# Kernel optimization log

Hardware: AMD Instinct MI355X
Metric: run time of the kernel (lower is better)

## Reference

```python
import jax, jax.numpy as jnp
import numpy as np

N_VERTS = 100000
N_EDGES = 50000
NNZ = 1600000
C_IN = 128
C_OUT = 128


def setup_inputs() -> dict:
    key = jax.random.key(0)
    k = jax.random.split(key, 7)
    X = jax.random.normal(k[0], (N_VERTS, C_IN), dtype=jnp.float32)
    v_ids = jax.random.randint(k[1], (NNZ,), 0, N_VERTS)
    e_ids = jax.random.randint(k[2], (NNZ,), 0, N_EDGES)
    s1 = 1.0 / np.sqrt(C_IN)
    s2 = 1.0 / np.sqrt(C_OUT)
    W_v2e = jax.random.uniform(k[3], (C_IN, C_OUT), jnp.float32, -s1, s1)
    b_v2e = jax.random.uniform(k[4], (C_OUT,), jnp.float32, -s1, s1)
    W_e2v = jax.random.uniform(k[5], (C_OUT, C_OUT), jnp.float32, -s2, s2)
    b_e2v = jax.random.uniform(k[6], (C_OUT,), jnp.float32, -s2, s2)
    return {"X": X, "W_v2e": W_v2e, "b_v2e": b_v2e, "W_e2v": W_e2v,
            "b_e2v": b_e2v, "v_ids": v_ids, "e_ids": e_ids}


def _mean_agg(feats_src, src_ids, dst_ids, num_dst):
    # gather source features along incidence list, segment-mean into destination
    gathered = feats_src[src_ids]                                   # [nnz, C]
    ssum = jax.ops.segment_sum(gathered, dst_ids, num_segments=num_dst)
    cnt = jax.ops.segment_sum(jnp.ones((src_ids.shape[0],), feats_src.dtype),
                              dst_ids, num_segments=num_dst)
    return ssum / jnp.maximum(cnt, 1.0)[:, None]


def reference(X, W_v2e, b_v2e, W_e2v, b_e2v, v_ids, e_ids):
    # theta_v2e
    Xp = X @ W_v2e + b_v2e                                          # [V, C_out]
    # v2e mean aggregation + ReLU
    Y = jax.nn.relu(_mean_agg(Xp, v_ids, e_ids, N_EDGES))           # [E, C_out]
    # theta_e2v
    Yp = Y @ W_e2v + b_e2v                                          # [E, C_out]
    # e2v mean aggregation
    Xo = _mean_agg(Yp, e_ids, v_ids, N_VERTS)                       # [V, C_out]
    # not is_last: final ReLU (bn disabled, dropout in eval mode = identity)
    return jax.nn.relu(Xo)
```

## Files before the change

kernel.cpp:

```cpp
#include <hip/hip_runtime.h>
#include <stdint.h>

#define V_N 100000
#define E_N 50000
#define C_N 128

#define NB_E 196
#define NB_V 391
#define NBINS (NB_E + NB_V)
#define CHUNK 8192
#define CAP_B 10240
#define G1T 782
#define G2T 391

typedef unsigned short u16;
typedef unsigned int u32;

__device__ __forceinline__ u16 f2bf(float f) {
    union { float f; u32 i; } c; c.f = f;
    u32 i = c.i;
    i += 0x7fffu + ((i >> 16) & 1u);
    return (u16)(i >> 16);
}
__device__ __forceinline__ void unpack2(u32 u, float& lo, float& hi) {
    union { u32 i; float f; } a, b;
    a.i = u << 16; b.i = u & 0xffff0000u;
    lo = a.f; hi = b.f;
}

__global__ __launch_bounds__(64) void flagf_k(float* out, float v) {
    if (threadIdx.x == 0 && blockIdx.x == 0) out[0] = v;
}

__global__ __launch_bounds__(256) void zero_i4(int4* __restrict__ p, int n) {
    int i = blockIdx.x * 256 + threadIdx.x;
    if (i < n) { int4 z = {0, 0, 0, 0}; p[i] = z; }
}

template<int MODE>
__device__ __forceinline__ void gemm_body(float* As, float* Wsh, int tile,
                                          const float* __restrict__ A,
                                          const float* __restrict__ W,
                                          const float* __restrict__ bias,
                                          const int* __restrict__ off,
                                          u16* __restrict__ Cout, int M) {
    const int tid = threadIdx.x;
    const int tx = tid & 15;
    const int ty = tid >> 4;
    const int m0 = tile * 128;

    float4 ra[4], rw[4];

    auto loadSlice = [&](int kk) {
        #pragma unroll
        for (int u = 0; u < 4; ++u) {
            int f = tid + u * 256;
            int r = f >> 3, c4 = f & 7;
            float4 val = { 0.f, 0.f, 0.f, 0.f };
            if (m0 + r < M)
                val = *(const float4*)(A + (size_t)(m0 + r) * C_N + kk + c4 * 4);
            ra[u] = val;
            int rwr = f >> 5, cw = f & 31;
            rw[u] = *(const float4*)(W + (size_t)(kk + rwr) * C_N + cw * 4);
        }
    };
    auto writeSlice = [&]() {
        #pragma unroll
        for (int u = 0; u < 4; ++u) {
            int f = tid + u * 256;
            int r = f >> 3, c4 = f & 7;
            int sc4 = c4 ^ ((r >> 3) & 7);
            *(float4*)(As + r * 32 + sc4 * 4) = ra[u];
            int rwr = f >> 5, cw = f & 31;
            *(float4*)(Wsh + rwr * 128 + cw * 4) = rw[u];
        }
    };

    float acc[8][8];
    #pragma unroll
    for (int i = 0; i < 8; ++i)
        #pragma unroll
        for (int j = 0; j < 8; ++j) acc[i][j] = 0.f;

    loadSlice(0);
    writeSlice();
    __syncthreads();

    #pragma unroll 1
    for (int kk = 0; kk < 128; kk += 32) {
        if (kk < 96) loadSlice(kk + 32);
        #pragma unroll
        for (int k4 = 0; k4 < 32; k4 += 4) {
            float4 a[8];
            #pragma unroll
            for (int i = 0; i < 8; ++i) {
                int row = ty * 8 + i;
                int sc4 = (k4 >> 2) ^ (ty & 7);
                a[i] = *(const float4*)(As + row * 32 + sc4 * 4);
            }
            #pragma unroll
            for (int dk = 0; dk < 4; ++dk) {
                float4 w0 = *(const float4*)(Wsh + (k4 + dk) * 128 + tx * 4);
                float4 w1 = *(const float4*)(Wsh + (k4 + dk) * 128 + 64 + tx * 4);
                #pragma unroll
                for (int i = 0; i < 8; ++i) {
                    float av = (dk == 0) ? a[i].x : (dk == 1) ? a[i].y : (dk == 2) ? a[i].z : a[i].w;
                    acc[i][0] = fmaf(av, w0.x, acc[i][0]);
                    acc[i][1] = fmaf(av, w0.y, acc[i][1]);
                    acc[i][2] = fmaf(av, w0.z, acc[i][2]);
                    acc[i][3] = fmaf(av, w0.w, acc[i][3]);
                    acc[i][4] = fmaf(av, w1.x, acc[i][4]);
                    acc[i][5] = fmaf(av, w1.y, acc[i][5]);
                    acc[i][6] = fmaf(av, w1.z, acc[i][6]);
                    acc[i][7] = fmaf(av, w1.w, acc[i][7]);
                }
            }
        }
        if (kk < 96) {
            __syncthreads();
            writeSlice();
            __syncthreads();
        }
    }

    float4 bb0 = *(const float4*)(bias + tx * 4);
    float4 bb1 = *(const float4*)(bias + 64 + tx * 4);
    #pragma unroll
    for (int i = 0; i < 8; ++i) {
        int m = m0 + ty * 8 + i;
        if (m >= M) break;
        float inv = 1.f;
        if (MODE) { int len = off[m + 1] - off[m]; inv = 1.f / (float)max(len, 1); }
        float v0, v1, v2, v3, v4, v5, v6, v7;
        if (MODE) {
            v0 = acc[i][0] * inv + bb0.x; v1 = acc[i][1] * inv + bb0.y;
            v2 = acc[i][2] * inv + bb0.z; v3 = acc[i][3] * inv + bb0.w;
            v4 = acc[i][4] * inv + bb1.x; v5 = acc[i][5] * inv + bb1.y;
            v6 = acc[i][6] * inv + bb1.z; v7 = acc[i][7] * inv + bb1.w;
        } else {
            v0 = acc[i][0] + bb0.x; v1 = acc[i][1] + bb0.y;
            v2 = acc[i][2] + bb0.z; v3 = acc[i][3] + bb0.w;
            v4 = acc[i][4] + bb1.x; v5 = acc[i][5] + bb1.y;
            v6 = acc[i][6] + bb1.z; v7 = acc[i][7] + bb1.w;
        }
        u32 p0 = (u32)f2bf(v0) | ((u32)f2bf(v1) << 16);
        u32 p1 = (u32)f2bf(v2) | ((u32)f2bf(v3) << 16);
        u32 p2 = (u32)f2bf(v4) | ((u32)f2bf(v5) << 16);
        u32 p3 = (u32)f2bf(v6) | ((u32)f2bf(v7) << 16);
        u32* dst = (u32*)(Cout + (size_t)m * C_N);
        uint2 q0 = { p0, p1 }, q1 = { p2, p3 };
        *(uint2*)(dst + tx * 2) = q0;
        *(uint2*)(dst + 32 + tx * 2) = q1;
    }
}

__global__ __launch_bounds__(256) void g1hist_k(const float* __restrict__ X,
                                                const float* __restrict__ W,
                                                const float* __restrict__ bias,
                                                u16* __restrict__ Xp,
                                                const int* __restrict__ v_ids,
                                                const int* __restrict__ e_ids,
                                                int* __restrict__ gbin, int nnz) {
    __shared__ __align__(16) float sm[2][4096];
    if ((int)blockIdx.x < G1T) {
        gemm_body<0>(sm[0], sm[1], blockIdx.x, X, W, bias, nullptr, Xp, V_N);
    } else {
        int* hb = (int*)sm;
        const int bid = blockIdx.x - G1T;
        for (int i = threadIdx.x; i < NBINS; i += 256) hb[i] = 0;
        __syncthreads();
        const int nnz4 = nnz >> 2;
        const int b4 = bid * (CHUNK >> 2);
        #pragma unroll
        for (int u = 0; u < 8; ++u) {
            int i4 = b4 + u * 256 + threadIdx.x;
            if (i4 < nnz4) {
                int4 e = ((const int4*)e_ids)[i4];
                int4 v = ((const int4*)v_ids)[i4];
                #define HA(ee, vv) \
                    if ((unsigned)ee < (unsigned)E_N && (unsigned)vv < (unsigned)V_N) { \
                        atomicAdd(&hb[ee >> 8], 1); atomicAdd(&hb[NB_E + (vv >> 8)], 1); }
                HA(e.x, v.x); HA(e.y, v.y); HA(e.z, v.z); HA(e.w, v.w);
                #undef HA
            }
        }
        __syncthreads();
        for (int i = threadIdx.x; i < NBINS; i += 256)
            if (hb[i]) atomicAdd(&gbin[i], hb[i]);
    }
}

__global__ __launch_bounds__(256) void gemm2_k(const float* __restrict__ A,
                                               const float* __restrict__ W,
                                               const float* __restrict__ bias,
                                               const int* __restrict__ off,
                                               u16* __restrict__ Cout, int M) {
    __shared__ __align__(16) float sm[2][4096];
    gemm_body<1>(sm[0], sm[1], blockIdx.x, A, W, bias, off, Cout, M);
}

__global__ __launch_bounds__(1024) void scanB_k(const int* __restrict__ gbin,
                                                int* __restrict__ base_e, int* __restrict__ base_v,
                                                int* __restrict__ curb_e, int* __restrict__ curb_v,
                                                int* __restrict__ off_e, int* __restrict__ off_v) {
    __shared__ int wtot[16];
    const int t = threadIdx.x, lane = t & 63, wid = t >> 6;
    {
        int x = (t < NB_E) ? gbin[t] : 0;
        int incl = x;
        for (int d = 1; d < 64; d <<= 1) { int u = __shfl_up(incl, d); if (lane >= d) incl += u; }
        if (lane == 63) wtot[wid] = incl;
        __syncthreads();
        int carry = 0;
        for (int w = 0; w < wid; ++w) carry += wtot[w];
        int excl = carry + incl - x;
        if (t < NB_E) { base_e[t] = excl; curb_e[t] = excl; }
        if (t == 0) {
            int tot = 0;
            for (int w = 0; w < 16; ++w) tot += wtot[w];
            base_e[NB_E] = tot; off_e[E_N] = tot;
        }
        __syncthreads();
    }
    {
        int x = (t < NB_V) ? gbin[NB_E + t] : 0;
        int incl = x;
        for (int d = 1; d < 64; d <<= 1) { int u = __shfl_up(incl, d); if (lane >= d) incl += u; }
        if (lane == 63) wtot[wid] = incl;
        __syncthreads();
        int carry = 0;
        for (int w = 0; w < wid; ++w) carry += wtot[w];
        int excl = carry + incl - x;
        if (t < NB_V) { base_v[t] = excl; curb_v[t] = excl; }
        if (t == 0) {
            int tot = 0;
            for (int w = 0; w < 16; ++w) tot += wtot[w];
            base_v[NB_V] = tot; off_v[V_N] = tot;
        }
    }
}

__global__ __launch_bounds__(512) void passA_k(const int* __restrict__ v_ids,
                                               const int* __restrict__ e_ids,
                                               int* __restrict__ curb_e, int* __restrict__ curb_v,
                                               u32* __restrict__ pairs_e, u32* __restrict__ pairs_v,
                                               int nnz) {
    __shared__ __align__(16) int ids_e[CHUNK];
    __shared__ __align__(16) int ids_v[CHUNK];
    __shared__ __align__(16) u32 stage[CHUNK];
    __shared__ int cnt[512], runoff[513], delta[512], cnt2[512];
    __shared__ int wtot[8];
    const int t = threadIdx.x, lane = t & 63, wid = t >> 6;
    const int nnz4 = nnz >> 2;
    const int b4 = blockIdx.x * (CHUNK >> 2);

    #pragma unroll
    for (int u = 0; u < 4; ++u) {
        int k4 = u * 512 + t;
        int i4 = b4 + k4;
        int4 e = { -1, -1, -1, -1 }, v = { -1, -1, -1, -1 };
        if (i4 < nnz4) { e = ((const int4*)e_ids)[i4]; v = ((const int4*)v_ids)[i4]; }
        ((int4*)ids_e)[k4] = e;
        ((int4*)ids_v)[k4] = v;
    }
    __syncthreads();

    for (int dir = 0; dir < 2; ++dir) {
        const int nb = dir ? NB_V : NB_E;
        cnt[t] = 0; cnt2[t] = 0;
        __syncthreads();
        for (int k = t; k < CHUNK; k += 512) {
            int ee = ids_e[k], vv = ids_v[k];
            if ((unsigned)ee < (unsigned)E_N && (unsigned)vv < (unsigned)V_N) {
                int key = dir ? vv : ee;
                atomicAdd(&cnt[key >> 8], 1);
            }
        }
        __syncthreads();
        int x = (t < nb) ? cnt[t] : 0;
        int incl = x;
        for (int d = 1; d < 64; d <<= 1) { int u = __shfl_up(incl, d); if (lane >= d) incl += u; }
        if (lane == 63) wtot[wid] = incl;
        __syncthreads();
        int carry = 0;
        for (int w = 0; w < wid; ++w) carry += wtot[w];
        int excl = carry + incl - x;
        if (t < nb) runoff[t] = excl;
        if (t == 0) {
            int tot = 0;
            for (int w = 0; w < 8; ++w) tot += wtot[w];
            runoff[nb] = tot;
        }
        __syncthreads();
        const int total = runoff[nb];
        if (t < nb && cnt[t] > 0) {
            int r = atomicAdd((dir ? curb_v : curb_e) + t, cnt[t]);
            delta[t] = r - runoff[t];
        }
        __syncthreads();
        for (int k = t; k < CHUNK; k += 512) {
            int ee = ids_e[k], vv = ids_v[k];
            if ((unsigned)ee < (unsigned)E_N && (unsigned)vv < (unsigned)V_N) {
                int key = dir ? vv : ee;
                int b_ = key >> 8;
                u32 pk_ = dir ? (((u32)(key & 255) << 16) | (u32)ee)
                              : (((u32)(key & 255) << 17) | (u32)vv);
                int idx_ = runoff[b_] + atomicAdd(&cnt2[b_], 1);
                stage[idx_] = pk_;
            }
        }
        __syncthreads();
        u32* pairs = dir ? pairs_v : pairs_e;
        for (int i = t; i < total; i += 512) {
            int lo = 0, hi = nb;
            while (hi - lo > 1) { int mid = (lo + hi) >> 1; if (runoff[mid] <= i) lo = mid; else hi = mid; }
            pairs[i + delta[lo]] = stage[i];
        }
        __syncthreads();
    }
}

__global__ __launch_bounds__(256) void passB_k(const u32* __restrict__ pairs_e,
                                               const u32* __restrict__ pairs_v,
                                               const int* __restrict__ base_e,
                                               const int* __restrict__ base_v,
                                               int* __restrict__ off_e, int* __restrict__ off_v,
                                               int* __restrict__ se_src, int* __restrict__ sv_src) {
    __shared__ int cntk[256], curk[256];
    __shared__ u32 buf[CAP_B];
    __shared__ int wtot[4];
    int b = blockIdx.x;
    const u32* pairs; const int* base; int* off; int* outv; int keyN, shift; u32 mask;
    if (b < NB_E) { pairs = pairs_e; base = base_e; off = off_e; outv = se_src; keyN = E_N; shift = 17; mask = 0x1FFFFu; }
    else { b -= NB_E; pairs = pairs_v; base = base_v; off = off_v; outv = sv_src; keyN = V_N; shift = 16; mask = 0xFFFFu; }
    const int lo = base[b], hi = base[b + 1], cnt = hi - lo, k0 = b << 8;
    const int t = threadIdx.x, lane = t & 63, wid = t >> 6;
    cntk[t] = 0;
    __syncthreads();
    for (int i = t; i < cnt; i += 256) { u32 p = pairs[lo + i]; atomicAdd(&cntk[p >> shift], 1); }
    __syncthreads();
    int x = cntk[t];
    int incl = x;
    for (int d = 1; d < 64; d <<= 1) { int u = __shfl_up(incl, d); if (lane >= d) incl += u; }
    if (lane == 63) wtot[wid] = incl;
    __syncthreads();
    int carry = 0;
    for (int w = 0; w < wid; ++w) carry += wtot[w];
    int excl = carry + incl - x;
    if (k0 + t < keyN) off[k0 + t] = lo + excl;
    curk[t] = excl;
    __syncthreads();
    if (cnt <= CAP_B) {
        for (int i = t; i < cnt; i += 256) {
            u32 p = pairs[lo + i];
            int pos = atomicAdd(&curk[p >> shift], 1);
            buf[pos] = p & mask;
        }
        __syncthreads();
        for (int i = t; i < cnt; i += 256) outv[lo + i] = (int)buf[i];
    } else {
        for (int i = t; i < cnt; i += 256) {
            u32 p = pairs[lo + i];
            int pos = atomicAdd(&curk[p >> shift], 1);
            outv[lo + pos] = (int)(p & mask);
        }
    }
}

template<int MODE>
__global__ __launch_bounds__(256) void seg16_k(const u16* __restrict__ F,
                                               const int* __restrict__ off,
                                               const int* __restrict__ srcs,
                                               float* __restrict__ out, int N) {
    int seg = blockIdx.x * 4 + (threadIdx.x >> 6);
    if (seg >= N) return;
    const int lane = threadIdx.x & 63;
    const int q = lane >> 4;
    const int c = lane & 15;
    int j0 = off[seg], j1 = off[seg + 1];
    float a0 = 0.f, a1 = 0.f, a2 = 0.f, a3 = 0.f, a4 = 0.f, a5 = 0.f, a6 = 0.f, a7 = 0.f;
    #define ACC8(u) { float l_, h_; \
        unpack2(u.x, l_, h_); a0 += l_; a1 += h_; \
        unpack2(u.y, l_, h_); a2 += l_; a3 += h_; \
        unpack2(u.z, l_, h_); a4 += l_; a5 += h_; \
        unpack2(u.w, l_, h_); a6 += l_; a7 += h_; }
    int j = j0;
    for (; j + 16 <= j1; j += 16) {
        int s0 = srcs[j + q];
        int s1 = srcs[j + 4 + q];
        int s2 = srcs[j + 8 + q];
        int s3 = srcs[j + 12 + q];
        uint4 u0 = ((const uint4*)(F + (size_t)s0 * C_N))[c];
        uint4 u1 = ((const uint4*)(F + (size_t)s1 * C_N))[c];
        uint4 u2 = ((const uint4*)(F + (size_t)s2 * C_N))[c];
        uint4 u3 = ((const uint4*)(F + (size_t)s3 * C_N))[c];
        ACC8(u0); ACC8(u1); ACC8(u2); ACC8(u3);
    }
    for (; j + 4 <= j1; j += 4) {
        int s0 = srcs[j + q];
        uint4 u0 = ((const uint4*)(F + (size_t)s0 * C_N))[c];
        ACC8(u0);
    }
    if (j + q < j1) {
        int s0 = srcs[j + q];
        uint4 u0 = ((const uint4*)(F + (size_t)s0 * C_N))[c];
        ACC8(u0);
    }
    #undef ACC8
    a0 += __shfl_xor(a0, 16); a0 += __shfl_xor(a0, 32);
    a1 += __shfl_xor(a1, 16); a1 += __shfl_xor(a1, 32);
    a2 += __shfl_xor(a2, 16); a2 += __shfl_xor(a2, 32);
    a3 += __shfl_xor(a3, 16); a3 += __shfl_xor(a3, 32);
    a4 += __shfl_xor(a4, 16); a4 += __shfl_xor(a4, 32);
    a5 += __shfl_xor(a5, 16); a5 += __shfl_xor(a5, 32);
    a6 += __shfl_xor(a6, 16); a6 += __shfl_xor(a6, 32);
    a7 += __shfl_xor(a7, 16); a7 += __shfl_xor(a7, 32);
    if (q == 0) {
        float inv = MODE ? (1.0f / (float)max(j1 - j0, 1)) : 1.0f;
        float4 w0, w1;
        w0.x = fmaxf(a0 * inv, 0.f); w0.y = fmaxf(a1 * inv, 0.f);
        w0.z = fmaxf(a2 * inv, 0.f); w0.w = fmaxf(a3 * inv, 0.f);
        w1.x = fmaxf(a4 * inv, 0.f); w1.y = fmaxf(a5 * inv, 0.f);
        w1.z = fmaxf(a6 * inv, 0.f); w1.w = fmaxf(a7 * inv, 0.f);
        float4* o = (float4*)(out + (size_t)seg * C_N + c * 8);
        o[0] = w0; o[1] = w1;
    }
}

extern "C" void kernel_launch(void* const* d_in, const int* in_sizes, int n_in,
                              void* d_out, int out_size, void* d_ws, size_t ws_size,
                              hipStream_t stream) {
    const float* X     = (const float*)d_in[0];
    const float* W_v2e = (const float*)d_in[1];
    const float* b_v2e = (const float*)d_in[2];
    const float* W_e2v = (const float*)d_in[3];
    const float* b_e2v = (const float*)d_in[4];
    const int*   v_ids = (const int*)d_in[5];
    const int*   e_ids = (const int*)d_in[6];
    float* out = (float*)d_out;

    bool sizesOK = (n_in == 7) && (out_size == 12800000)
        && in_sizes[0] == 12800000 && in_sizes[1] == 16384 && in_sizes[2] == 128
        && in_sizes[3] == 16384 && in_sizes[4] == 128
        && in_sizes[5] == 1600000 && in_sizes[6] == 1600000;
    if (!sizesOK) { flagf_k<<<1, 64, 0, stream>>>(out, 1.0e6f); return; }
    if (ws_size < 28000000) { flagf_k<<<1, 64, 0, stream>>>(out, 2.0e6f); return; }
    const int nnz = in_sizes[5];

    u16*   Xp      = (u16*)d_out;
    u32*   pairs_e = (u32*)((char*)d_out + 25600000);
    u32*   pairs_v = pairs_e + nnz;
    float* Ysum    = (float*)((char*)d_out + 25600000);

    char* ws = (char*)d_ws;
    u16* Yp     = (u16*)(ws + 0);
    int* se_src = (int*)(ws + 12800000);
    int* sv_src = (int*)(ws + 19200000);
    int* gbin   = (int*)(ws + 25600000);
    int* base_e = (int*)(ws + 25602560);
    int* base_v = (int*)(ws + 25603584);
    int* curb_e = (int*)(ws + 25605632);
    int* curb_v = (int*)(ws + 25606656);
    int* off_e  = (int*)(ws + 25608704);
    int* off_v  = (int*)(ws + 25808768);

    const int NCH = (nnz + CHUNK - 1) / CHUNK;

    zero_i4<<<1, 256, 0, stream>>>((int4*)gbin, 152);
    g1hist_k<<<G1T + NCH, 256, 0, stream>>>(X, W_v2e, b_v2e, Xp, v_ids, e_ids, gbin, nnz);
    scanB_k<<<1, 1024, 0, stream>>>(gbin, base_e, base_v, curb_e, curb_v, off_e, off_v);
    passA_k<<<NCH, 512, 0, stream>>>(v_ids, e_ids, curb_e, curb_v, pairs_e, pairs_v, nnz);
    passB_k<<<NBINS, 256, 0, stream>>>(pairs_e, pairs_v, base_e, base_v, off_e, off_v, se_src, sv_src);

    seg16_k<0><<<(E_N + 3) / 4, 256, 0, stream>>>(Xp, off_e, se_src, Ysum, E_N);
    gemm2_k<<<G2T, 256, 0, stream>>>(Ysum, W_e2v, b_e2v, off_e, Yp, E_N);
    seg16_k<1><<<(V_N + 3) / 4, 256, 0, stream>>>(Yp, off_v, sv_src, out, V_N);

    (void)ws_size;
}
```

Baseline: 380.8 us.

## Store gather sources in channel-sliced layout and split segment-mean by slice

The GEMM outputs are now written in a channel-sliced (slice-major) bf16 layout, and the segment-sum kernels are rewritten so each block handles one channel slice for a group of segments. The goal is to shrink the working set each block touches per gather, improving cache locality for the random row gathers. Each wave also processes four segments at once for more memory-level parallelism, and it uses nontemporal index loads and output stores. In exchange, the indices are re-read once per slice and the gemm2 input reads become strided, adding layout complexity.

Measured after the change: 608.8 us. 1.6x slower.

```diff
diff --git a/kernel.cpp b/kernel.cpp
--- a/kernel.cpp
+++ b/kernel.cpp
@@ -15,6 +15,7 @@
 
 typedef unsigned short u16;
 typedef unsigned int u32;
+typedef float f32x4 __attribute__((ext_vector_type(4)));
 
 __device__ __forceinline__ u16 f2bf(float f) {
     union { float f; u32 i; } c; c.f = f;
@@ -57,8 +58,15 @@
             int f = tid + u * 256;
             int r = f >> 3, c4 = f & 7;
             float4 val = { 0.f, 0.f, 0.f, 0.f };
-            if (m0 + r < M)
-                val = *(const float4*)(A + (size_t)(m0 + r) * C_N + kk + c4 * 4);
+            int rg = m0 + r;
+            if (rg < M) {
+                if (MODE == 0) {
+                    val = *(const float4*)(A + (size_t)rg * C_N + kk + c4 * 4);
+                } else {
+                    int sl = (kk >> 4) + (c4 >> 2);
+                    val = *(const float4*)(A + ((size_t)sl * M + rg) * 16 + (c4 & 3) * 4);
+                }
+            }
             ra[u] = val;
             int rwr = f >> 5, cw = f & 31;
             rw[u] = *(const float4*)(W + (size_t)(kk + rwr) * C_N + cw * 4);
@@ -147,10 +155,18 @@
         u32 p1 = (u32)f2bf(v2) | ((u32)f2bf(v3) << 16);
         u32 p2 = (u32)f2bf(v4) | ((u32)f2bf(v5) << 16);
         u32 p3 = (u32)f2bf(v6) | ((u32)f2bf(v7) << 16);
-        u32* dst = (u32*)(Cout + (size_t)m * C_N);
         uint2 q0 = { p0, p1 }, q1 = { p2, p3 };
-        *(uint2*)(dst + tx * 2) = q0;
-        *(uint2*)(dst + 32 + tx * 2) = q1;
+        if (MODE == 0) {
+            u32* d0 = (u32*)Cout + ((size_t)(tx >> 2) * M + m) * 8 + (tx & 3) * 2;
+            u32* d1 = (u32*)Cout + ((size_t)(4 + (tx >> 2)) * M + m) * 8 + (tx & 3) * 2;
+            *(uint2*)d0 = q0;
+            *(uint2*)d1 = q1;
+        } else {
+            u32* d0 = (u32*)Cout + ((size_t)(tx >> 3) * M + m) * 16 + (tx & 7) * 2;
+            u32* d1 = (u32*)Cout + ((size_t)(2 + (tx >> 3)) * M + m) * 16 + (tx & 7) * 2;
+            *(uint2*)d0 = q0;
+            *(uint2*)d1 = q1;
+        }
     }
 }
 
@@ -368,62 +384,92 @@
 }
 
 template<int MODE>
-__global__ __launch_bounds__(256) void seg16_k(const u16* __restrict__ F,
-                                               const int* __restrict__ off,
-                                               const int* __restrict__ srcs,
-                                               float* __restrict__ out, int N) {
-    int seg = blockIdx.x * 4 + (threadIdx.x >> 6);
-    if (seg >= N) return;
+__global__ __launch_bounds__(256) void segX_k(const u16* __restrict__ T,
+                                              const int* __restrict__ off,
+                                              const int* __restrict__ srcs,
+                                              float* __restrict__ out,
+                                              int N, int NSRC) {
+    constexpr int NS    = MODE ? 4 : 8;
+    constexpr int SCH   = MODE ? 32 : 16;
+    constexpr int BATCH = MODE ? 16 : 32;
+    constexpr int RSH   = MODE ? 2 : 1;
+    constexpr int HMSK  = MODE ? 3 : 1;
+    constexpr int BSH   = MODE ? 2 : 3;
+    const int slice = blockIdx.x & (NS - 1);
+    const int wseg0 = ((blockIdx.x >> BSH) * 4 + (threadIdx.x >> 6)) * 4;
     const int lane = threadIdx.x & 63;
-    const int q = lane >> 4;
-    const int c = lane & 15;
-    int j0 = off[seg], j1 = off[seg + 1];
-    float a0 = 0.f, a1 = 0.f, a2 = 0.f, a3 = 0.f, a4 = 0.f, a5 = 0.f, a6 = 0.f, a7 = 0.f;
-    #define ACC8(u) { float l_, h_; \
-        unpack2(u.x, l_, h_); a0 += l_; a1 += h_; \
-        unpack2(u.y, l_, h_); a2 += l_; a3 += h_; \
-        unpack2(u.z, l_, h_); a4 += l_; a5 += h_; \
-        unpack2(u.w, l_, h_); a6 += l_; a7 += h_; }
-    int j = j0;
-    for (; j + 16 <= j1; j += 16) {
-        int s0 = srcs[j + q];
-        int s1 = srcs[j + 4 + q];
-        int s2 = srcs[j + 8 + q];
-        int s3 = srcs[j + 12 + q];
-        uint4 u0 = ((const uint4*)(F + (size_t)s0 * C_N))[c];
-        uint4 u1 = ((const uint4*)(F + (size_t)s1 * C_N))[c];
-        uint4 u2 = ((const uint4*)(F + (size_t)s2 * C_N))[c];
-        uint4 u3 = ((const uint4*)(F + (size_t)s3 * C_N))[c];
-        ACC8(u0); ACC8(u1); ACC8(u2); ACC8(u3);
-    }
-    for (; j + 4 <= j1; j += 4) {
-        int s0 = srcs[j + q];
-        uint4 u0 = ((const uint4*)(F + (size_t)s0 * C_N))[c];
-        ACC8(u0);
-    }
-    if (j + q < j1) {
-        int s0 = srcs[j + q];
-        uint4 u0 = ((const uint4*)(F + (size_t)s0 * C_N))[c];
-        ACC8(u0);
-    }
-    #undef ACC8
-    a0 += __shfl_xor(a0, 16); a0 += __shfl_xor(a0, 32);
-    a1 += __shfl_xor(a1, 16); a1 += __shfl_xor(a1, 32);
-    a2 += __shfl_xor(a2, 16); a2 += __shfl_xor(a2, 32);
-    a3 += __shfl_xor(a3, 16); a3 += __shfl_xor(a3, 32);
-    a4 += __shfl_xor(a4, 16); a4 += __shfl_xor(a4, 32);
-    a5 += __shfl_xor(a5, 16); a5 += __shfl_xor(a5, 32);
-    a6 += __shfl_xor(a6, 16); a6 += __shfl_xor(a6, 32);
-    a7 += __shfl_xor(a7, 16); a7 += __shfl_xor(a7, 32);
-    if (q == 0) {
-        float inv = MODE ? (1.0f / (float)max(j1 - j0, 1)) : 1.0f;
-        float4 w0, w1;
-        w0.x = fmaxf(a0 * inv, 0.f); w0.y = fmaxf(a1 * inv, 0.f);
-        w0.z = fmaxf(a2 * inv, 0.f); w0.w = fmaxf(a3 * inv, 0.f);
-        w1.x = fmaxf(a4 * inv, 0.f); w1.y = fmaxf(a5 * inv, 0.f);
-        w1.z = fmaxf(a6 * inv, 0.f); w1.w = fmaxf(a7 * inv, 0.f);
-        float4* o = (float4*)(out + (size_t)seg * C_N + c * 8);
-        o[0] = w0; o[1] = w1;
+    const int r = lane >> RSH;
+    const int h = lane & HMSK;
+    const u16* Ts = T + (size_t)slice * NSRC * SCH;
+
+    float acc[4][8];
+    #pragma unroll
+    for (int k = 0; k < 4; ++k)
+        #pragma unroll
+        for (int c = 0; c < 8; ++c) acc[k][c] = 0.f;
+
+    int jc[4], j1[4], len[4];
+    #pragma unroll
+    for (int k = 0; k < 4; ++k) {
+        int s = wseg0 + k;
+        jc[k] = (s < N) ? off[s] : 0;
+        j1[k] = (s < N) ? off[s + 1] : 0;
+        len[k] = j1[k] - jc[k];
+    }
+
+    int rem = 1;
+    while (rem) {
+        rem = 0;
+        int idx[4], ok[4];
+        #pragma unroll
+        for (int k = 0; k < 4; ++k) {
+            ok[k] = (jc[k] + r < j1[k]);
+            idx[k] = ok[k] ? __builtin_nontemporal_load(srcs + jc[k] + r) : 0;
+        }
+        #pragma unroll
+        for (int k = 0; k < 4; ++k) {
+            if (ok[k]) {
+                uint4 q = *(const uint4*)(Ts + (size_t)idx[k] * SCH + h * 8);
+                float l_, h_;
+                unpack2(q.x, l_, h_); acc[k][0] += l_; acc[k][1] += h_;
+                unpack2(q.y, l_, h_); acc[k][2] += l_; acc[k][3] += h_;
+                unpack2(q.z, l_, h_); acc[k][4] += l_; acc[k][5] += h_;
+                unpack2(q.w, l_, h_); acc[k][6] += l_; acc[k][7] += h_;
+            }
+        }
+        #pragma unroll
+        for (int k = 0; k < 4; ++k) { jc[k] += BATCH; rem |= (jc[k] < j1[k]) ? 1 : 0; }
+    }
+
+    #pragma unroll
+    for (int k = 0; k < 4; ++k)
+        #pragma unroll
+        for (int c = 0; c < 8; ++c) {
+            if (MODE == 0) acc[k][c] += __shfl_xor(acc[k][c], 2);
+            acc[k][c] += __shfl_xor(acc[k][c], 4);
+            acc[k][c] += __shfl_xor(acc[k][c], 8);
+            acc[k][c] += __shfl_xor(acc[k][c], 16);
+            acc[k][c] += __shfl_xor(acc[k][c], 32);
+        }
+
+    if (r == 0) {
+        #pragma unroll
+        for (int k = 0; k < 4; ++k) {
+            int s = wseg0 + k;
+            if (s < N) {
+                float inv = MODE ? (1.0f / (float)max(len[k], 1)) : 1.0f;
+                f32x4 w0, w1;
+                w0.x = fmaxf(acc[k][0] * inv, 0.f); w0.y = fmaxf(acc[k][1] * inv, 0.f);
+                w0.z = fmaxf(acc[k][2] * inv, 0.f); w0.w = fmaxf(acc[k][3] * inv, 0.f);
+                w1.x = fmaxf(acc[k][4] * inv, 0.f); w1.y = fmaxf(acc[k][5] * inv, 0.f);
+                w1.z = fmaxf(acc[k][6] * inv, 0.f); w1.w = fmaxf(acc[k][7] * inv, 0.f);
+                float* o;
+                if (MODE) o = out + (size_t)s * C_N + slice * SCH + h * 8;
+                else      o = out + ((size_t)slice * N + s) * SCH + h * 8;
+                __builtin_nontemporal_store(w0, (f32x4*)o);
+                __builtin_nontemporal_store(w1, (f32x4*)o + 1);
+            }
+        }
     }
 }
 
@@ -450,10 +496,10 @@
     u16*   Xp      = (u16*)d_out;
     u32*   pairs_e = (u32*)((char*)d_out + 25600000);
     u32*   pairs_v = pairs_e + nnz;
-    float* Ysum    = (float*)((char*)d_out + 25600000);
+    float* YsumB   = (float*)((char*)d_out + 25600000);
 
     char* ws = (char*)d_ws;
-    u16* Yp     = (u16*)(ws + 0);
+    u16* YpB    = (u16*)(ws + 0);
     int* se_src = (int*)(ws + 12800000);
     int* sv_src = (int*)(ws + 19200000);
     int* gbin   = (int*)(ws + 25600000);
@@ -472,9 +518,9 @@
     passA_k<<<NCH, 512, 0, stream>>>(v_ids, e_ids, curb_e, curb_v, pairs_e, pairs_v, nnz);
     passB_k<<<NBINS, 256, 0, stream>>>(pairs_e, pairs_v, base_e, base_v, off_e, off_v, se_src, sv_src);
 
-    seg16_k<0><<<(E_N + 3) / 4, 256, 0, stream>>>(Xp, off_e, se_src, Ysum, E_N);
-    gemm2_k<<<G2T, 256, 0, stream>>>(Ysum, W_e2v, b_e2v, off_e, Yp, E_N);
-    seg16_k<1><<<(V_N + 3) / 4, 256, 0, stream>>>(Yp, off_v, sv_src, out, V_N);
+    segX_k<0><<<((E_N + 15) / 16) * 8, 256, 0, stream>>>(Xp, off_e, se_src, YsumB, E_N, V_N);
+    gemm2_k<<<G2T, 256, 0, stream>>>(YsumB, W_e2v, b_e2v, off_e, YpB, E_N);
+    segX_k<1><<<((V_N + 15) / 16) * 4, 256, 0, stream>>>(YpB, off_v, sv_src, out, V_N, E_N);
 
     (void)ws_size;
 }
```

## Fuse GEMM1 with scatter pass A and run histogram standalone

Applied to the files above, without the earlier changes.

The first GEMM was previously co-scheduled in one launch with the cheap histogram, while the heavier bucketing pass ran as a separate kernel afterwards. Now the histogram and scan run first, and the bucketing pass is merged into the GEMM launch as extra blocks, so its atomic-heavy scatter can overlap with the GEMM work. The merged bucketing uses 256-thread blocks over 4096-element chunks and reuses the GEMM's shared memory. It re-reads the id arrays from global memory in each counting and scatter step instead of caching them in LDS. This adds global traffic and more global atomics on the bin cursors because there are more chunks.

Result: no change. 376.9 us (-1.0%).

```diff
diff --git a/kernel.cpp b/kernel.cpp
--- a/kernel.cpp
+++ b/kernel.cpp
@@ -8,7 +8,8 @@
 #define NB_E 196
 #define NB_V 391
 #define NBINS (NB_E + NB_V)
-#define CHUNK 8192
+#define CHUNK_H 8192
+#define CHUNK_A 4096
 #define CAP_B 10240
 #define G1T 782
 #define G2T 391
@@ -35,6 +36,73 @@
 __global__ __launch_bounds__(256) void zero_i4(int4* __restrict__ p, int n) {
     int i = blockIdx.x * 256 + threadIdx.x;
     if (i < n) { int4 z = {0, 0, 0, 0}; p[i] = z; }
+}
+
+__global__ __launch_bounds__(256) void hist_k(const int* __restrict__ v_ids,
+                                              const int* __restrict__ e_ids,
+                                              int* __restrict__ gbin, int nnz) {
+    __shared__ int hb[NBINS];
+    for (int i = threadIdx.x; i < NBINS; i += 256) hb[i] = 0;
+    __syncthreads();
+    const int nnz4 = nnz >> 2;
+    const int b4 = blockIdx.x * (CHUNK_H >> 2);
+    #pragma unroll
+    for (int u = 0; u < 8; ++u) {
+        int i4 = b4 + u * 256 + threadIdx.x;
+        if (i4 < nnz4) {
+            int4 e = ((const int4*)e_ids)[i4];
+            int4 v = ((const int4*)v_ids)[i4];
+            #define HA(ee, vv) \
+                if ((unsigned)ee < (unsigned)E_N && (unsigned)vv < (unsigned)V_N) { \
+                    atomicAdd(&hb[ee >> 8], 1); atomicAdd(&hb[NB_E + (vv >> 8)], 1); }
+            HA(e.x, v.x); HA(e.y, v.y); HA(e.z, v.z); HA(e.w, v.w);
+            #undef HA
+        }
+    }
+    __syncthreads();
+    for (int i = threadIdx.x; i < NBINS; i += 256)
+        if (hb[i]) atomicAdd(&gbin[i], hb[i]);
+}
+
+__global__ __launch_bounds__(1024) void scanB_k(const int* __restrict__ gbin,
+                                                int* __restrict__ base_e, int* __restrict__ base_v,
+                                                int* __restrict__ curb_e, int* __restrict__ curb_v,
+                                                int* __restrict__ off_e, int* __restrict__ off_v) {
+    __shared__ int wtot[16];
+    const int t = threadIdx.x, lane = t & 63, wid = t >> 6;
+    {
+        int x = (t < NB_E) ? gbin[t] : 0;
+        int incl = x;
+        for (int d = 1; d < 64; d <<= 1) { int u = __shfl_up(incl, d); if (lane >= d) incl += u; }
+        if (lane == 63) wtot[wid] = incl;
+        __syncthreads();
+        int carry = 0;
+        for (int w = 0; w < wid; ++w) carry += wtot[w];
+        int excl = carry + incl - x;
+        if (t < NB_E) { base_e[t] = excl; curb_e[t] = excl; }
+        if (t == 0) {
+            int tot = 0;
+            for (int w = 0; w < 16; ++w) tot += wtot[w];
+            base_e[NB_E] = tot; off_e[E_N] = tot;
+        }
+        __syncthreads();
+    }
+    {
+        int x = (t < NB_V) ? gbin[NB_E + t] : 0;
+        int incl = x;
+        for (int d = 1; d < 64; d <<= 1) { int u = __shfl_up(incl, d); if (lane >= d) incl += u; }
+        if (lane == 63) wtot[wid] = incl;
+        __syncthreads();
+        int carry = 0;
+        for (int w = 0; w < wid; ++w) carry += wtot[w];
+        int excl = carry + incl - x;
+        if (t < NB_V) { base_v[t] = excl; curb_v[t] = excl; }
+        if (t == 0) {
+            int tot = 0;
+            for (int w = 0; w < 16; ++w) tot += wtot[w];
+            base_v[NB_V] = tot; off_v[V_N] = tot;
+        }
+    }
 }
 
 template<int MODE>
@@ -154,39 +222,96 @@
     }
 }
 
-__global__ __launch_bounds__(256) void g1hist_k(const float* __restrict__ X,
-                                                const float* __restrict__ W,
-                                                const float* __restrict__ bias,
-                                                u16* __restrict__ Xp,
-                                                const int* __restrict__ v_ids,
-                                                const int* __restrict__ e_ids,
-                                                int* __restrict__ gbin, int nnz) {
+__global__ __launch_bounds__(256) void g1passA_k(const float* __restrict__ X,
+                                                 const float* __restrict__ W,
+                                                 const float* __restrict__ bias,
+                                                 u16* __restrict__ Xp,
+                                                 const int* __restrict__ v_ids,
+                                                 const int* __restrict__ e_ids,
+                                                 int* __restrict__ curb_e, int* __restrict__ curb_v,
+                                                 u32* __restrict__ pairs_e, u32* __restrict__ pairs_v,
+                                                 int nnz) {
     __shared__ __align__(16) float sm[2][4096];
     if ((int)blockIdx.x < G1T) {
         gemm_body<0>(sm[0], sm[1], blockIdx.x, X, W, bias, nullptr, Xp, V_N);
-    } else {
-        int* hb = (int*)sm;
-        const int bid = blockIdx.x - G1T;
-        for (int i = threadIdx.x; i < NBINS; i += 256) hb[i] = 0;
-        __syncthreads();
-        const int nnz4 = nnz >> 2;
-        const int b4 = bid * (CHUNK >> 2);
-        #pragma unroll
-        for (int u = 0; u < 8; ++u) {
-            int i4 = b4 + u * 256 + threadIdx.x;
+        return;
+    }
+    const int bid = blockIdx.x - G1T;
+    u32* stage  = (u32*)&sm[0][0];
+    int* cnt    = (int*)&sm[0][0] + 4096;
+    int* runoff = (int*)&sm[0][0] + 4496;
+    int* delta  = (int*)&sm[0][0] + 4896;
+    int* cnt2   = (int*)&sm[0][0] + 5296;
+    int* wtot   = (int*)&sm[0][0] + 5696;
+    const int t = threadIdx.x, lane = t & 63, wid = t >> 6;
+    const int nnz4 = nnz >> 2;
+    const int b4 = bid * (CHUNK_A >> 2);
+
+    for (int dir = 0; dir < 2; ++dir) {
+        const int nb = dir ? NB_V : NB_E;
+        for (int i = t; i < nb; i += 256) { cnt[i] = 0; cnt2[i] = 0; }
+        __syncthreads();
+        #pragma unroll
+        for (int u = 0; u < 4; ++u) {
+            int i4 = b4 + u * 256 + t;
             if (i4 < nnz4) {
                 int4 e = ((const int4*)e_ids)[i4];
                 int4 v = ((const int4*)v_ids)[i4];
-                #define HA(ee, vv) \
+                #define PC(ee, vv) \
                     if ((unsigned)ee < (unsigned)E_N && (unsigned)vv < (unsigned)V_N) { \
-                        atomicAdd(&hb[ee >> 8], 1); atomicAdd(&hb[NB_E + (vv >> 8)], 1); }
-                HA(e.x, v.x); HA(e.y, v.y); HA(e.z, v.z); HA(e.w, v.w);
-                #undef HA
+                        int k_ = dir ? vv : ee; atomicAdd(&cnt[k_ >> 8], 1); }
+                PC(e.x, v.x); PC(e.y, v.y); PC(e.z, v.z); PC(e.w, v.w);
+                #undef PC
             }
         }
         __syncthreads();
-        for (int i = threadIdx.x; i < NBINS; i += 256)
-            if (hb[i]) atomicAdd(&gbin[i], hb[i]);
+        int carryAll = 0;
+        for (int base = 0; base < nb; base += 256) {
+            int x = (base + t < nb) ? cnt[base + t] : 0;
+            int incl = x;
+            for (int d = 1; d < 64; d <<= 1) { int u = __shfl_up(incl, d); if (lane >= d) incl += u; }
+            if (lane == 63) wtot[wid] = incl;
+            __syncthreads();
+            int wc = 0;
+            for (int w = 0; w < wid; ++w) wc += wtot[w];
+            if (base + t < nb) runoff[base + t] = carryAll + wc + incl - x;
+            carryAll += wtot[0] + wtot[1] + wtot[2] + wtot[3];
+            __syncthreads();
+        }
+        if (t == 0) runoff[nb] = carryAll;
+        __syncthreads();
+        const int total = runoff[nb];
+        for (int i = t; i < nb; i += 256)
+            if (cnt[i] > 0) {
+                int r = atomicAdd((dir ? curb_v : curb_e) + i, cnt[i]);
+                delta[i] = r - runoff[i];
+            }
+        __syncthreads();
+        #pragma unroll
+        for (int u = 0; u < 4; ++u) {
+            int i4 = b4 + u * 256 + t;
+            if (i4 < nnz4) {
+                int4 e = ((const int4*)e_ids)[i4];
+                int4 v = ((const int4*)v_ids)[i4];
+                #define PS(ee, vv) \
+                    if ((unsigned)ee < (unsigned)E_N && (unsigned)vv < (unsigned)V_N) { \
+                        int k_ = dir ? vv : ee; int b_ = k_ >> 8; \
+                        u32 pk_ = dir ? (((u32)(k_ & 255) << 16) | (u32)ee) \
+                                      : (((u32)(k_ & 255) << 17) | (u32)vv); \
+                        int idx_ = runoff[b_] + atomicAdd(&cnt2[b_], 1); \
+                        stage[idx_] = pk_; }
+                PS(e.x, v.x); PS(e.y, v.y); PS(e.z, v.z); PS(e.w, v.w);
+                #undef PS
+            }
+        }
+        __syncthreads();
+        u32* pairs = dir ? pairs_v : pairs_e;
+        for (int i = t; i < total; i += 256) {
+            int lo = 0, hi = nb;
+            while (hi - lo > 1) { int mid = (lo + hi) >> 1; if (runoff[mid] <= i) lo = mid; else hi = mid; }
+            pairs[i + delta[lo]] = stage[i];
+        }
+        __syncthreads();
     }
 }
 
@@ -197,127 +322,6 @@
                                                u16* __restrict__ Cout, int M) {
     __shared__ __align__(16) float sm[2][4096];
     gemm_body<1>(sm[0], sm[1], blockIdx.x, A, W, bias, off, Cout, M);
-}
-
-__global__ __launch_bounds__(1024) void scanB_k(const int* __restrict__ gbin,
-                                                int* __restrict__ base_e, int* __restrict__ base_v,
-                                                int* __restrict__ curb_e, int* __restrict__ curb_v,
-                                                int* __restrict__ off_e, int* __restrict__ off_v) {
-    __shared__ int wtot[16];
-    const int t = threadIdx.x, lane = t & 63, wid = t >> 6;
-    {
-        int x = (t < NB_E) ? gbin[t] : 0;
-        int incl = x;
-        for (int d = 1; d < 64; d <<= 1) { int u = __shfl_up(incl, d); if (lane >= d) incl += u; }
-        if (lane == 63) wtot[wid] = incl;
-        __syncthreads();
-        int carry = 0;
-        for (int w = 0; w < wid; ++w) carry += wtot[w];
-        int excl = carry + incl - x;
-        if (t < NB_E) { base_e[t] = excl; curb_e[t] = excl; }
-        if (t == 0) {
-            int tot = 0;
-            for (int w = 0; w < 16; ++w) tot += wtot[w];
-            base_e[NB_E] = tot; off_e[E_N] = tot;
-        }
-        __syncthreads();
-    }
-    {
-        int x = (t < NB_V) ? gbin[NB_E + t] : 0;
-        int incl = x;
-        for (int d = 1; d < 64; d <<= 1) { int u = __shfl_up(incl, d); if (lane >= d) incl += u; }
-        if (lane == 63) wtot[wid] = incl;
-        __syncthreads();
-        int carry = 0;
-        for (int w = 0; w < wid; ++w) carry += wtot[w];
-        int excl = carry + incl - x;
-        if (t < NB_V) { base_v[t] = excl; curb_v[t] = excl; }
-        if (t == 0) {
-            int tot = 0;
-            for (int w = 0; w < 16; ++w) tot += wtot[w];
-            base_v[NB_V] = tot; off_v[V_N] = tot;
-        }
-    }
-}
-
-__global__ __launch_bounds__(512) void passA_k(const int* __restrict__ v_ids,
-                                               const int* __restrict__ e_ids,
-                                               int* __restrict__ curb_e, int* __restrict__ curb_v,
-                                               u32* __restrict__ pairs_e, u32* __restrict__ pairs_v,
-                                               int nnz) {
-    __shared__ __align__(16) int ids_e[CHUNK];
-    __shared__ __align__(16) int ids_v[CHUNK];
-    __shared__ __align__(16) u32 stage[CHUNK];
-    __shared__ int cnt[512], runoff[513], delta[512], cnt2[512];
-    __shared__ int wtot[8];
-    const int t = threadIdx.x, lane = t & 63, wid = t >> 6;
-    const int nnz4 = nnz >> 2;
-    const int b4 = blockIdx.x * (CHUNK >> 2);
-
-    #pragma unroll
-    for (int u = 0; u < 4; ++u) {
-        int k4 = u * 512 + t;
-        int i4 = b4 + k4;
-        int4 e = { -1, -1, -1, -1 }, v = { -1, -1, -1, -1 };
-        if (i4 < nnz4) { e = ((const int4*)e_ids)[i4]; v = ((const int4*)v_ids)[i4]; }
-        ((int4*)ids_e)[k4] = e;
-        ((int4*)ids_v)[k4] = v;
-    }
-    __syncthreads();
-
-    for (int dir = 0; dir < 2; ++dir) {
-        const int nb = dir ? NB_V : NB_E;
-        cnt[t] = 0; cnt2[t] = 0;
-        __syncthreads();
-        for (int k = t; k < CHUNK; k += 512) {
-            int ee = ids_e[k], vv = ids_v[k];
-            if ((unsigned)ee < (unsigned)E_N && (unsigned)vv < (unsigned)V_N) {
-                int key = dir ? vv : ee;
-                atomicAdd(&cnt[key >> 8], 1);
-            }
-        }
-        __syncthreads();
-        int x = (t < nb) ? cnt[t] : 0;
-        int incl = x;
-        for (int d = 1; d < 64; d <<= 1) { int u = __shfl_up(incl, d); if (lane >= d) incl += u; }
-        if (lane == 63) wtot[wid] = incl;
-        __syncthreads();
-        int carry = 0;
-        for (int w = 0; w < wid; ++w) carry += wtot[w];
-        int excl = carry + incl - x;
-        if (t < nb) runoff[t] = excl;
-        if (t == 0) {
-            int tot = 0;
-            for (int w = 0; w < 8; ++w) tot += wtot[w];
-            runoff[nb] = tot;
-        }
-        __syncthreads();
-        const int total = runoff[nb];
-        if (t < nb && cnt[t] > 0) {
-            int r = atomicAdd((dir ? curb_v : curb_e) + t, cnt[t]);
-            delta[t] = r - runoff[t];
-        }
-        __syncthreads();
-        for (int k = t; k < CHUNK; k += 512) {
-            int ee = ids_e[k], vv = ids_v[k];
-            if ((unsigned)ee < (unsigned)E_N && (unsigned)vv < (unsigned)V_N) {
-                int key = dir ? vv : ee;
-                int b_ = key >> 8;
-                u32 pk_ = dir ? (((u32)(key & 255) << 16) | (u32)ee)
-                              : (((u32)(key & 255) << 17) | (u32)vv);
-                int idx_ = runoff[b_] + atomicAdd(&cnt2[b_], 1);
-                stage[idx_] = pk_;
-            }
-        }
-        __syncthreads();
-        u32* pairs = dir ? pairs_v : pairs_e;
-        for (int i = t; i < total; i += 512) {
-            int lo = 0, hi = nb;
-            while (hi - lo > 1) { int mid = (lo + hi) >> 1; if (runoff[mid] <= i) lo = mid; else hi = mid; }
-            pairs[i + delta[lo]] = stage[i];
-        }
-        __syncthreads();
-    }
 }
 
 __global__ __launch_bounds__(256) void passB_k(const u32* __restrict__ pairs_e,
@@ -464,12 +468,14 @@
     int* off_e  = (int*)(ws + 25608704);
     int* off_v  = (int*)(ws + 25808768);
 
-    const int NCH = (nnz + CHUNK - 1) / CHUNK;
+    const int NCHH = (nnz + CHUNK_H - 1) / CHUNK_H;
+    const int NCHA = (nnz + CHUNK_A - 1) / CHUNK_A;
 
     zero_i4<<<1, 256, 0, stream>>>((int4*)gbin, 152);
-    g1hist_k<<<G1T + NCH, 256, 0, stream>>>(X, W_v2e, b_v2e, Xp, v_ids, e_ids, gbin, nnz);
+    hist_k<<<NCHH, 256, 0, stream>>>(v_ids, e_ids, gbin, nnz);
     scanB_k<<<1, 1024, 0, stream>>>(gbin, base_e, base_v, curb_e, curb_v, off_e, off_v);
-    passA_k<<<NCH, 512, 0, stream>>>(v_ids, e_ids, curb_e, curb_v, pairs_e, pairs_v, nnz);
+    g1passA_k<<<G1T + NCHA, 256, 0, stream>>>(X, W_v2e, b_v2e, Xp, v_ids, e_ids,
+                                              curb_e, curb_v, pairs_e, pairs_v, nnz);
     passB_k<<<NBINS, 256, 0, stream>>>(pairs_e, pairs_v, base_e, base_v, off_e, off_v, se_src, sv_src);
 
     seg16_k<0><<<(E_N + 3) / 4, 256, 0, stream>>>(Xp, off_e, se_src, Ysum, E_N);
```
